# Performance work log

Measured on AMD Instinct MI355X. Metric: run time of the kernel, lower is better.

The kernel has to match this reference:

```python
import jax, jax.numpy as jnp
import numpy as np
from jax import lax


def binarize(x):
    # tf.sign with 0 mapped to +1
    return jnp.where(x >= 0, jnp.ones_like(x), -jnp.ones_like(x))


def setup_inputs() -> dict:
    key = jax.random.key(0)
    kx, kw = jax.random.split(key)
    x = jax.random.normal(kx, (64, 56, 56, 128), dtype=jnp.float32)
    # weights init: normal stddev=0.1, shape (kh, kw, in_ch, filters) == HWIO
    w = jax.random.normal(kw, (3, 3, 128, 256), dtype=jnp.float32) * 0.1
    return {"x": x, "w": w}


def reference(x, w):
    x_bin = binarize(x)
    w_bin = binarize(w)
    # NHWC input, HWIO kernel, SAME padding, stride (1,1)
    out = lax.conv_general_dilated(
        x_bin, w_bin,
        window_strides=(1, 1),
        padding="SAME",
        dimension_numbers=("NHWC", "HWIO", "NHWC"),
    )
    return out
```

## Files before the change

kernel.cpp:

```cpp
#include <hip/hip_runtime.h>
#include <stdint.h>


#define IH 56
#define IW 56
#define CIN 128
#define COUT 256
#define NB 64

__global__ void pack_x_kernel(const float* __restrict__ x,
                              uint64_t* __restrict__ xp, int npix) {
    int gtid = blockIdx.x * blockDim.x + threadIdx.x;
    int wave = gtid >> 6, lane = gtid & 63;
    int nw = (gridDim.x * blockDim.x) >> 6;
    const float2* x2 = (const float2*)x;
    for (int p = wave; p < npix; p += nw) {
        float2 v = x2[(size_t)p * 64 + lane];
        uint64_t m0 = __ballot(v.x < 0.0f);
        uint64_t m1 = __ballot(v.y < 0.0f);
        if (lane == 0) { xp[2 * (size_t)p] = m0; xp[2 * (size_t)p + 1] = m1; }
    }
}

__global__ void pack_w_kernel(const float* __restrict__ w,
                              uint64_t* __restrict__ wp) {
    int gtid = blockIdx.x * blockDim.x + threadIdx.x;
    int wave = gtid >> 6, lane = gtid & 63;
    int nw = (gridDim.x * blockDim.x) >> 6;
    const int ntask = 9 * 2 * COUT;
    for (int t = wave; t < ntask; t += nw) {
        int oc = t & 255, hf = (t >> 8) & 1, tap = t >> 9;
        float v = w[((size_t)(tap * CIN + 2 * lane + hf)) * COUT + oc];
        uint64_t m = __ballot(v < 0.0f);
        if (lane == 0) wp[(size_t)(tap * 2 + hf) * COUT + oc] = m;
    }
}

__device__ __forceinline__ void tap2(const uint64_t c[2], const uint64_t w[2][2],
                                     int& a, int& b) {
    a += __popcll(c[0] ^ w[0][0]) + __popcll(c[1] ^ w[1][0]);
    b += __popcll(c[0] ^ w[0][1]) + __popcll(c[1] ^ w[1][1]);
}

__device__ __forceinline__ void popc9x2(const uint64_t X[3][2], const uint64_t Y[3][2],
                                        const uint64_t Z[3][2],
                                        const uint64_t wr[9][2][2], int& a, int& b) {
#pragma unroll
    for (int kh = 0; kh < 3; ++kh) {
        tap2(X[kh], wr[kh * 3 + 0], a, b);
        tap2(Y[kh], wr[kh * 3 + 1], a, b);
        tap2(Z[kh], wr[kh * 3 + 2], a, b);
    }
}

#define LOADCOL(dst, cc)                                        \
    do {                                                        \
        _Pragma("unroll")                                       \
        for (int _k = 0; _k < 3; ++_k) {                        \
            ulonglong2 _t = *(const ulonglong2*)xs[cc][g + _k]; \
            dst[_k][0] = _t.x; dst[_k][1] = _t.y;               \
        }                                                       \
    } while (0)

#define STEP(Xc, Yc, Zc, Kk)                                     \
    do {                                                         \
        int _a = 0, _b = 0;                                      \
        popc9x2(Xc, Yc, Zc, wr, _a, _b);                         \
        float2 _o;                                               \
        _o.x = (float)(Kk[0] - 2 * _a);                          \
        _o.y = (float)(Kk[1] - 2 * _b);                          \
        *(float2*)po = _o;                                       \
        po += COUT;                                              \
    } while (0)

__global__ __launch_bounds__(256, 2) void bconv_kernel(
        const uint64_t* __restrict__ xp,
        const uint64_t* __restrict__ wp,
        float* __restrict__ out) {
    __shared__ alignas(16) uint64_t xs[58][4][2];

    int bh = blockIdx.x % 28;
    int n  = blockIdx.x / 28;
    int h0 = bh * 2;
    int tid = threadIdx.x;
    int g = tid >> 7;
    int q = tid & 127;
    int oc0 = 2 * q;
    int h = h0 + g;

    for (int i = tid; i < 4 * 58; i += 256) {
        int row = i / 58, col = i % 58;
        int rr = h0 - 1 + row, cc = col - 1;
        uint64_t v0 = 0, v1 = 0;
        if ((unsigned)rr < IH && (unsigned)cc < IW) {
            const uint64_t* pp = xp + 2 * (((size_t)n * IH + rr) * IW + cc);
            v0 = pp[0]; v1 = pp[1];
        }
        xs[col][row][0] = v0; xs[col][row][1] = v1;
    }

    uint64_t wr[9][2][2];
#pragma unroll
    for (int t = 0; t < 9; ++t) {
#pragma unroll
        for (int hf = 0; hf < 2; ++hf) {
            ulonglong2 v = *(const ulonglong2*)&wp[(size_t)(t * 2 + hf) * COUT + oc0];
            wr[t][hf][0] = v.x; wr[t][hf][1] = v.y;
        }
    }
    __syncthreads();

    int pc[2][9];
#pragma unroll
    for (int t = 0; t < 9; ++t) {
        pc[0][t] = __popcll(wr[t][0][0]) + __popcll(wr[t][1][0]);
        pc[1][t] = __popcll(wr[t][0][1]) + __popcll(wr[t][1][1]);
    }
    bool e0 = (h == 0), e2 = (h == IH - 1);
    int K0a[2], Kia[2], K55a[2];
#pragma unroll
    for (int s = 0; s < 2; ++s) {
        int rs0 = pc[s][0] + pc[s][1] + pc[s][2];
        int rs2 = pc[s][6] + pc[s][7] + pc[s][8];
        int cs0 = pc[s][0] + pc[s][3] + pc[s][6];
        int cs2 = pc[s][2] + pc[s][5] + pc[s][8];
        int vh  = 3 - (e0 ? 1 : 0) - (e2 ? 1 : 0);
        int inv = e0 ? rs0 : (e2 ? rs2 : 0);
        int c0  = e0 ? pc[s][0] : (e2 ? pc[s][6] : 0);
        int c2  = e0 ? pc[s][2] : (e2 ? pc[s][8] : 0);
        Kia[s]  = 384 * vh + 2 * inv;
        K0a[s]  = 256 * vh + 2 * (inv + cs0 - c0);
        K55a[s] = 256 * vh + 2 * (inv + cs2 - c2);
    }

    float* po = out + (((size_t)n * IH + h) * IW) * COUT + oc0;

    uint64_t A[3][2], B[3][2], C[3][2];
    LOADCOL(A, 0);
    LOADCOL(B, 1);
    LOADCOL(C, 2);
    STEP(A, B, C, K0a);
    LOADCOL(A, 3);
    STEP(B, C, A, Kia);
    for (int wb = 2; wb <= 53; wb += 3) {
        LOADCOL(B, wb + 2);
        STEP(C, A, B, Kia);
        LOADCOL(C, wb + 3);
        STEP(A, B, C, Kia);
        LOADCOL(A, wb + 4);
        if (wb == 53) { STEP(B, C, A, K55a); }
        else          { STEP(B, C, A, Kia); }
    }
}

extern "C" void kernel_launch(void* const* d_in, const int* in_sizes, int n_in,
                              void* d_out, int out_size, void* d_ws, size_t ws_size,
                              hipStream_t stream) {
    const float* x = (const float*)d_in[0];
    const float* w = (const float*)d_in[1];
    float* out = (float*)d_out;

    uint64_t* wp = (uint64_t*)d_ws;
    uint64_t* xp = (uint64_t*)((char*)d_ws + (64 << 10));

    const int npix = NB * IH * IW;

    pack_x_kernel<<<6272, 256, 0, stream>>>(x, xp, npix);
    pack_w_kernel<<<288, 256, 0, stream>>>(w, wp);
    bconv_kernel<<<NB * 28, 256, 0, stream>>>(xp, wp, out);
}
```

Baseline: 369.7 us.

## Replace popcount binary conv with int8 MFMA on 0/1 expanded bits

```diff
diff --git a/kernel.cpp b/kernel.cpp
--- a/kernel.cpp
+++ b/kernel.cpp
@@ -4,9 +4,14 @@
 
 #define IH 56
 #define IW 56
-#define CIN 128
 #define COUT 256
 #define NB 64
+#define ROWPX 58
+#define PXB 144
+#define ROWB (ROWPX * PXB)
+
+typedef int v4i  __attribute__((ext_vector_type(4)));
+typedef int v16i __attribute__((ext_vector_type(16)));
 
 __global__ void pack_x_kernel(const float* __restrict__ x,
                               uint64_t* __restrict__ xp, int npix) {
@@ -30,126 +35,161 @@
     const int ntask = 9 * 2 * COUT;
     for (int t = wave; t < ntask; t += nw) {
         int oc = t & 255, hf = (t >> 8) & 1, tap = t >> 9;
-        float v = w[((size_t)(tap * CIN + 2 * lane + hf)) * COUT + oc];
+        float v = w[((size_t)(tap * 128 + 2 * lane + hf)) * COUT + oc];
         uint64_t m = __ballot(v < 0.0f);
         if (lane == 0) wp[(size_t)(tap * 2 + hf) * COUT + oc] = m;
     }
 }
 
-__device__ __forceinline__ void tap2(const uint64_t c[2], const uint64_t w[2][2],
-                                     int& a, int& b) {
-    a += __popcll(c[0] ^ w[0][0]) + __popcll(c[1] ^ w[1][0]);
-    b += __popcll(c[0] ^ w[0][1]) + __popcll(c[1] ^ w[1][1]);
-}
-
-__device__ __forceinline__ void popc9x2(const uint64_t X[3][2], const uint64_t Y[3][2],
-                                        const uint64_t Z[3][2],
-                                        const uint64_t wr[9][2][2], int& a, int& b) {
-#pragma unroll
-    for (int kh = 0; kh < 3; ++kh) {
-        tap2(X[kh], wr[kh * 3 + 0], a, b);
-        tap2(Y[kh], wr[kh * 3 + 1], a, b);
-        tap2(Z[kh], wr[kh * 3 + 2], a, b);
-    }
-}
-
-#define LOADCOL(dst, cc)                                        \
-    do {                                                        \
-        _Pragma("unroll")                                       \
-        for (int _k = 0; _k < 3; ++_k) {                        \
-            ulonglong2 _t = *(const ulonglong2*)xs[cc][g + _k]; \
-            dst[_k][0] = _t.x; dst[_k][1] = _t.y;               \
-        }                                                       \
-    } while (0)
-
-#define STEP(Xc, Yc, Zc, Kk)                                     \
-    do {                                                         \
-        int _a = 0, _b = 0;                                      \
-        popc9x2(Xc, Yc, Zc, wr, _a, _b);                         \
-        float2 _o;                                               \
-        _o.x = (float)(Kk[0] - 2 * _a);                          \
-        _o.y = (float)(Kk[1] - 2 * _b);                          \
-        *(float2*)po = _o;                                       \
-        po += COUT;                                              \
-    } while (0)
-
-__global__ __launch_bounds__(256, 2) void bconv_kernel(
+__global__ void swz_w_kernel(const uint64_t* __restrict__ wp,
+                             char* __restrict__ bsw, int* __restrict__ kct) {
+    int t = blockIdx.x * blockDim.x + threadIdx.x;
+    if (t < 36 * 8 * 64) {
+        int lane = t & 63, ntks = t >> 6;
+        int nt = ntks & 7, ks = ntks >> 3;
+        int oc = nt * 32 + (lane & 31);
+        int kk = ks * 32 + (lane >> 5) * 16;
+        int tap = kk >> 7, c = kk & 127;
+        int hf = c >> 6, bit0 = c & 63;
+        uint64_t word = wp[(size_t)(tap * 2 + hf) * COUT + oc];
+        int4 d;
+        d.x = (int)(((uint32_t)(word >> (bit0 + 0))  & 0xF) * 0x00204081u & 0x01010101u);
+        d.y = (int)(((uint32_t)(word >> (bit0 + 4))  & 0xF) * 0x00204081u & 0x01010101u);
+        d.z = (int)(((uint32_t)(word >> (bit0 + 8))  & 0xF) * 0x00204081u & 0x01010101u);
+        d.w = (int)(((uint32_t)(word >> (bit0 + 12)) & 0xF) * 0x00204081u & 0x01010101u);
+        *(int4*)(bsw + (size_t)t * 16) = d;
+    } else if (t < 36 * 8 * 64 + 256) {
+        int oc = t - 36 * 8 * 64;
+        int Sw[9];
+#pragma unroll
+        for (int tp = 0; tp < 9; ++tp)
+            Sw[tp] = __popcll(wp[(size_t)(tp * 2) * COUT + oc]) +
+                     __popcll(wp[(size_t)(tp * 2 + 1) * COUT + oc]);
+        for (int hc = 0; hc < 3; ++hc)
+            for (int wc = 0; wc < 3; ++wc) {
+                int K = 0;
+                for (int kh = 0; kh < 3; ++kh) {
+                    if (hc == 0 && kh == 0) continue;
+                    if (hc == 2 && kh == 2) continue;
+                    for (int kw = 0; kw < 3; ++kw) {
+                        if (wc == 0 && kw == 0) continue;
+                        if (wc == 2 && kw == 2) continue;
+                        K += 128 - 2 * Sw[kh * 3 + kw];
+                    }
+                }
+                kct[(hc * 3 + wc) * COUT + oc] = K;
+            }
+    }
+}
+
+__global__ __launch_bounds__(256, 2) void bconv_mfma(
         const uint64_t* __restrict__ xp,
-        const uint64_t* __restrict__ wp,
+        const char* __restrict__ bsw,
+        const int* __restrict__ kct,
         float* __restrict__ out) {
-    __shared__ alignas(16) uint64_t xs[58][4][2];
-
-    int bh = blockIdx.x % 28;
-    int n  = blockIdx.x / 28;
-    int h0 = bh * 2;
+    __shared__ alignas(16) char xs8[4 * ROWB];
+    __shared__ int pc[4][ROWPX];
+    __shared__ int sx9[2][IW];
+
+    int bh = blockIdx.x % 28, n = blockIdx.x / 28;
+    int hbase = bh * 2;
     int tid = threadIdx.x;
-    int g = tid >> 7;
-    int q = tid & 127;
-    int oc0 = 2 * q;
-    int h = h0 + g;
-
-    for (int i = tid; i < 4 * 58; i += 256) {
-        int row = i / 58, col = i % 58;
-        int rr = h0 - 1 + row, cc = col - 1;
-        uint64_t v0 = 0, v1 = 0;
+
+    for (int t = tid; t < 4 * ROWPX; t += 256) {
+        int row = t / ROWPX, col = t % ROWPX;
+        int rr = hbase - 1 + row, cc = col - 1;
+        uint64_t w0 = 0, w1 = 0;
         if ((unsigned)rr < IH && (unsigned)cc < IW) {
             const uint64_t* pp = xp + 2 * (((size_t)n * IH + rr) * IW + cc);
-            v0 = pp[0]; v1 = pp[1];
+            w0 = pp[0]; w1 = pp[1];
         }
-        xs[col][row][0] = v0; xs[col][row][1] = v1;
-    }
-
-    uint64_t wr[9][2][2];
-#pragma unroll
-    for (int t = 0; t < 9; ++t) {
-#pragma unroll
-        for (int hf = 0; hf < 2; ++hf) {
-            ulonglong2 v = *(const ulonglong2*)&wp[(size_t)(t * 2 + hf) * COUT + oc0];
-            wr[t][hf][0] = v.x; wr[t][hf][1] = v.y;
+        pc[row][col] = __popcll(w0) + __popcll(w1);
+        uint32_t* dst = (uint32_t*)(xs8 + row * ROWB + col * PXB);
+#pragma unroll
+        for (int i = 0; i < 16; ++i)
+            dst[i] = ((uint32_t)(w0 >> (4 * i)) & 0xF) * 0x00204081u & 0x01010101u;
+#pragma unroll
+        for (int i = 0; i < 16; ++i)
+            dst[16 + i] = ((uint32_t)(w1 >> (4 * i)) & 0xF) * 0x00204081u & 0x01010101u;
+    }
+    __syncthreads();
+
+    for (int t = tid; t < 2 * IW; t += 256) {
+        int g = t / IW, px = t % IW;
+        int s = 0;
+#pragma unroll
+        for (int kh = 0; kh < 3; ++kh)
+            s += pc[g + kh][px] + pc[g + kh][px + 1] + pc[g + kh][px + 2];
+        sx9[g][px] = s;
+    }
+    __syncthreads();
+
+    int wv = tid >> 6, lane = tid & 63;
+    int g = wv >> 1;
+    int nt0 = (wv & 1) * 4;
+    int m = lane & 31, half = lane >> 5;
+
+    v16i acc[2][4];
+#pragma unroll
+    for (int mt = 0; mt < 2; ++mt)
+#pragma unroll
+        for (int j = 0; j < 4; ++j)
+#pragma unroll
+            for (int r = 0; r < 16; ++r) acc[mt][j][r] = 0;
+
+    const v4i* bbase = (const v4i*)bsw + (size_t)nt0 * 64 + lane;
+
+    for (int tap = 0; tap < 9; ++tap) {
+        int kh = tap / 3, kw = tap % 3;
+        const char* arow = xs8 + (g + kh) * ROWB + kw * PXB;
+#pragma unroll
+        for (int kc = 0; kc < 4; ++kc) {
+            int choff = kc * 32 + half * 16;
+            v4i a0 = *(const v4i*)(arow + (0  + m) * PXB + choff);
+            v4i a1 = *(const v4i*)(arow + (24 + m) * PXB + choff);
+            int ks = tap * 4 + kc;
+            const v4i* bp = bbase + (size_t)ks * 8 * 64;
+#pragma unroll
+            for (int j = 0; j < 4; ++j) {
+                v4i b = bp[j * 64];
+                acc[0][j] = __builtin_amdgcn_mfma_i32_32x32x32_i8(a0, b, acc[0][j], 0, 0, 0);
+                acc[1][j] = __builtin_amdgcn_mfma_i32_32x32x32_i8(a1, b, acc[1][j], 0, 0, 0);
+            }
         }
     }
-    __syncthreads();
-
-    int pc[2][9];
-#pragma unroll
-    for (int t = 0; t < 9; ++t) {
-        pc[0][t] = __popcll(wr[t][0][0]) + __popcll(wr[t][1][0]);
-        pc[1][t] = __popcll(wr[t][0][1]) + __popcll(wr[t][1][1]);
-    }
-    bool e0 = (h == 0), e2 = (h == IH - 1);
-    int K0a[2], Kia[2], K55a[2];
-#pragma unroll
-    for (int s = 0; s < 2; ++s) {
-        int rs0 = pc[s][0] + pc[s][1] + pc[s][2];
-        int rs2 = pc[s][6] + pc[s][7] + pc[s][8];
-        int cs0 = pc[s][0] + pc[s][3] + pc[s][6];
-        int cs2 = pc[s][2] + pc[s][5] + pc[s][8];
-        int vh  = 3 - (e0 ? 1 : 0) - (e2 ? 1 : 0);
-        int inv = e0 ? rs0 : (e2 ? rs2 : 0);
-        int c0  = e0 ? pc[s][0] : (e2 ? pc[s][6] : 0);
-        int c2  = e0 ? pc[s][2] : (e2 ? pc[s][8] : 0);
-        Kia[s]  = 384 * vh + 2 * inv;
-        K0a[s]  = 256 * vh + 2 * (inv + cs0 - c0);
-        K55a[s] = 256 * vh + 2 * (inv + cs2 - c2);
-    }
-
-    float* po = out + (((size_t)n * IH + h) * IW) * COUT + oc0;
-
-    uint64_t A[3][2], B[3][2], C[3][2];
-    LOADCOL(A, 0);
-    LOADCOL(B, 1);
-    LOADCOL(C, 2);
-    STEP(A, B, C, K0a);
-    LOADCOL(A, 3);
-    STEP(B, C, A, Kia);
-    for (int wb = 2; wb <= 53; wb += 3) {
-        LOADCOL(B, wb + 2);
-        STEP(C, A, B, Kia);
-        LOADCOL(C, wb + 3);
-        STEP(A, B, C, Kia);
-        LOADCOL(A, wb + 4);
-        if (wb == 53) { STEP(B, C, A, K55a); }
-        else          { STEP(B, C, A, Kia); }
+
+    int h = hbase + g;
+    int hc = (h == 0) ? 0 : ((h == IH - 1) ? 2 : 1);
+    float* orow = out + (((size_t)n * IH + h) * IW) * COUT;
+
+    int sxv[2][16];
+#pragma unroll
+    for (int r = 0; r < 16; ++r) {
+        int pxr = (r & 3) + 8 * (r >> 2) + 4 * half;
+        sxv[0][r] = sx9[g][pxr];
+        sxv[1][r] = sx9[g][24 + pxr];
+    }
+
+#pragma unroll
+    for (int j = 0; j < 4; ++j) {
+        int ocj = (nt0 + j) * 32 + m;
+        int Ki  = kct[(hc * 3 + 1) * COUT + ocj];
+        int K0  = kct[(hc * 3 + 0) * COUT + ocj];
+        int K55 = kct[(hc * 3 + 2) * COUT + ocj];
+#pragma unroll
+        for (int mt = 0; mt < 2; ++mt) {
+            int Mb = mt ? 24 : 0;
+#pragma unroll
+            for (int r = 0; r < 16; ++r) {
+                int pxr = (r & 3) + 8 * (r >> 2) + 4 * half;
+                int px = Mb + pxr;
+                int K = Ki;
+                if (mt == 0 && r == 0 && half == 0) K = K0;
+                if (mt == 1 && r == 15 && half == 1) K = K55;
+                float o = (float)(K - 2 * sxv[mt][r] + 4 * acc[mt][j][r]);
+                orow[(size_t)px * COUT + ocj] = o;
+            }
+        }
     }
 }
 
@@ -160,12 +200,15 @@
     const float* w = (const float*)d_in[1];
     float* out = (float*)d_out;
 
-    uint64_t* wp = (uint64_t*)d_ws;
-    uint64_t* xp = (uint64_t*)((char*)d_ws + (64 << 10));
+    uint64_t* wp  = (uint64_t*)d_ws;
+    int*      kct = (int*)((char*)d_ws + 36864);
+    char*     bsw = (char*)d_ws + 46080;
+    uint64_t* xp  = (uint64_t*)((char*)d_ws + 344064);
 
     const int npix = NB * IH * IW;
 
     pack_x_kernel<<<6272, 256, 0, stream>>>(x, xp, npix);
     pack_w_kernel<<<288, 256, 0, stream>>>(w, wp);
-    bconv_kernel<<<NB * 28, 256, 0, stream>>>(xp, wp, out);
-}
+    swz_w_kernel<<<73, 256, 0, stream>>>(wp, bsw, kct);
+    bconv_mfma<<<NB * 28, 256, 0, stream>>>(xp, bsw, kct, out);
+}
```

Measured after the change: 370.6 us. Within noise of the previous version (+0.3%).
